# Optimization experiments

Hardware: AMD Instinct MI355X
Metric: run time of the kernel (lower is better)

## Reference

```python
import jax, jax.numpy as jnp
import numpy as np

N_STATE = 12
HID = 128
BS = 16384


def setup_inputs() -> dict:
    key = jax.random.key(0)
    ks = jax.random.split(key, 16)
    s = 0.05
    inp = {
        'state': jax.random.normal(ks[0], (BS, N_STATE), dtype=jnp.float32),
        'safe_m': jax.random.uniform(ks[1], (N_STATE,), minval=0.5, maxval=2.0, dtype=jnp.float32),
        'safe_l': -jax.random.uniform(ks[2], (N_STATE,), minval=0.5, maxval=2.0, dtype=jnp.float32),
        'W0': jax.random.normal(ks[3], (HID, N_STATE), dtype=jnp.float32) * s,
        'b0': jax.random.normal(ks[4], (HID,), dtype=jnp.float32) * s,
        'W1': jax.random.normal(ks[5], (HID, HID), dtype=jnp.float32) * s,
        'b1': jax.random.normal(ks[6], (HID,), dtype=jnp.float32) * s,
        'W2': jax.random.normal(ks[7], (HID, HID), dtype=jnp.float32) * s,
        'b2': jax.random.normal(ks[8], (HID,), dtype=jnp.float32) * s,
        'W3': jax.random.normal(ks[9], (HID, HID), dtype=jnp.float32) * s,
        'b3': jax.random.normal(ks[10], (HID,), dtype=jnp.float32) * s,
        'Wout': jax.random.normal(ks[11], (1, HID), dtype=jnp.float32) * s,
        'bout': jax.random.normal(ks[12], (1,), dtype=jnp.float32) * s,
    }
    return inp


def _linear(V, JV, W, b):
    # V: (bs, in) -> (bs, out); JV: (bs, in, n) -> (bs, out, n)
    return V @ W.T + b, jnp.einsum('oh,bhn->bon', W, JV)


def _tanh(V, JV):
    V = jnp.tanh(V)
    # diag_embed(1 - V^2) @ JV  ==  elementwise row scaling
    return V, (1.0 - V * V)[:, :, None] * JV


def reference(state, safe_m, safe_l, W0, b0, W1, b1, W2, b2, W3, b3, Wout, bout):
    bs = state.shape[0]
    x_center = (safe_m + safe_l) * 0.5            # (n,)
    x_range = (safe_m - safe_l) * 0.5             # (n,)
    x_norm = (state - x_center) / x_range         # (bs, n)

    # JV initialized to diag(1/x_range), broadcast over batch
    JV = jnp.broadcast_to(jnp.diag(1.0 / x_range), (bs, N_STATE, N_STATE))

    V, JV = _linear(x_norm, JV, W0, b0)   # input_linear
    V, JV = _tanh(V, JV)                  # input_activation
    V, JV = _linear(V, JV, W1, b1)        # layer_0_linear
    V, JV = _tanh(V, JV)                  # layer_0_activation
    V, JV = _linear(V, JV, W2, b2)        # layer_1_linear
    V, JV = _tanh(V, JV)                  # layer_1_activation
    V, JV = _linear(V, JV, W3, b3)        # layer_2_linear (no activation)
    V, JV = _linear(V, JV, Wout, bout)    # output_linear -> V:(bs,1), JV:(bs,1,n)

    # HJH = hstack(h, Jh) generalized over batch: (bs, 1 + n_state)
    return jnp.concatenate([V, JV[:, 0, :]], axis=1)
```

## Files before the change

kernel.cpp:

```cpp
#include <hip/hip_runtime.h>

#define NS  12
#define HID 128
#define SPB 8
#define RB  128

typedef __attribute__((ext_vector_type(8))) short bf8_t;
typedef __attribute__((ext_vector_type(4))) float f4_t;

#define O_W0H 0
#define O_W0L 2048
#define O_WH(i) (4096 + (i) * 16384)
#define O_WL(i) (O_WH(i) + 8192)

__device__ __forceinline__ unsigned f2bf_u(float f) {
  unsigned u = __float_as_uint(f);
  return (u + 0x7FFFu + ((u >> 16) & 1u)) >> 16;
}
__device__ __forceinline__ float bf2f(unsigned h) { return __uint_as_float(h << 16); }

__device__ __forceinline__ unsigned cvtpk(float a, float b) {
  unsigned r;
  asm("v_cvt_pk_bf16_f32 %0, %1, %2" : "=v"(r) : "v"(a), "v"(b));
  return r;
}
__device__ __forceinline__ float fast_tanh(float v) {
  float vc = fminf(fmaxf(v, -15.f), 15.f);
  float e = __expf(vc + vc);
  return (e - 1.f) * __builtin_amdgcn_rcpf(e + 1.f);
}
__device__ __forceinline__ f4_t mfma16(bf8_t a, bf8_t b, f4_t c) {
  return __builtin_amdgcn_mfma_f32_16x16x32_bf16(a, b, c, 0, 0, 0);
}

__global__ __launch_bounds__(256) void prep_w(
    const float* __restrict__ W0, const float* __restrict__ W1,
    const float* __restrict__ W2, const float* __restrict__ W3,
    unsigned* __restrict__ ws)
{
  int t = blockIdx.x * 256 + threadIdx.x;
  if (t >= 53248) return;
  int tile = t >> 9;
  int pos  = t & 511;
  int g = pos >> 7, o = (pos >> 3) & 15, j = pos & 7;

  const float* src; int kdim; unsigned hoff, loff; int lt;
  if (tile < 8) { src = W0; kdim = NS; hoff = O_W0H; loff = O_W0L; lt = tile; }
  else {
    int li = (tile - 8) >> 5;  lt = (tile - 8) & 31;
    src = (li == 0) ? W1 : (li == 1) ? W2 : W3;
    kdim = HID; hoff = O_WH(li); loff = O_WL(li);
  }
  int ks = (tile < 8) ? 0 : (lt >> 3);
  int mt = (tile < 8) ? lt : (lt & 7);
  int k = ks * 32 + g * 8 + j;
  int orow = mt * 16 + o;
  float v = (k < kdim) ? src[orow * kdim + k] : 0.f;
  unsigned h = f2bf_u(v);
  unsigned lo = f2bf_u(v - bf2f(h));
  int idx = lt * 512 + pos;
  ((unsigned short*)(ws + hoff))[idx] = (unsigned short)h;
  ((unsigned short*)(ws + loff))[idx] = (unsigned short)lo;
}

template<int KSUBS, bool ACT>
__device__ __forceinline__ void layer(
    unsigned* __restrict__ S, const unsigned* __restrict__ whi,
    const unsigned* __restrict__ wlo, const float* __restrict__ bias,
    int lane, int l15, int g, int bp, int rwave, int mwave, int mt0)
{
  f4_t acc[4][2];
  #pragma unroll
  for (int a = 0; a < 4; ++a)
    #pragma unroll
    for (int b = 0; b < 2; ++b) acc[a][b] = (f4_t){0.f, 0.f, 0.f, 0.f};

  const int aswz = (l15 & 7) << 2;
  #pragma unroll
  for (int ks = 0; ks < KSUBS; ++ks) {
    bf8_t bh[2], bl[2];
    #pragma unroll
    for (int mm = 0; mm < 2; ++mm) {
      int tb = (ks * 8 + mt0 + mm) * 256 + lane * 4;
      bh[mm] = __builtin_bit_cast(bf8_t, *(const uint4*)(whi + tb));
      bl[mm] = __builtin_bit_cast(bf8_t, *(const uint4*)(wlo + tb));
    }
    #pragma unroll
    for (int rs = 0; rs < 4; ++rs) {
      int row = rwave + rs * 16 + l15;
      int idx = row * 64 + ((ks * 16 + g * 4) ^ aswz);
      bf8_t avh = __builtin_bit_cast(bf8_t, *(const uint4*)(S + idx));
      bf8_t avl = __builtin_bit_cast(bf8_t, *(const uint4*)(S + 8192 + idx));
      #pragma unroll
      for (int mm = 0; mm < 2; ++mm) {
        acc[rs][mm] = mfma16(avh, bh[mm], acc[rs][mm]);
        acc[rs][mm] = mfma16(avh, bl[mm], acc[rs][mm]);
        acc[rs][mm] = mfma16(avl, bh[mm], acc[rs][mm]);
      }
    }
  }
  __syncthreads();

  const bool even = (lane & 1) == 0;
  #pragma unroll
  for (int rs = 0; rs < 4; ++rs) {
    #pragma unroll
    for (int mm = 0; mm < 2; ++mm) {
      int col = mwave + mm * 16 + l15;
      float bv = bias[col];
      f4_t a = acc[rs][mm];
      int rb = rwave + rs * 16 + g * 4;
      if (ACT) {
        float vb = __int_as_float(__builtin_amdgcn_ds_bpermute(bp, __float_as_int(a[0])));
        float t = fast_tanh(vb + bv);
        float s = 1.f - t * t;
        a[0] = (g == 0) ? t : a[0] * s;
        a[1] *= s; a[2] *= s; a[3] *= s;
        int wc = col >> 1;
        #pragma unroll
        for (int j = 0; j < 4; ++j) {
          float pv = __shfl_xor(a[j], 1);
          float vlo = even ? a[j] : pv;
          float vhi = even ? pv : a[j];
          unsigned wh = cvtpk(vlo, vhi);
          float rl = vlo - __uint_as_float(wh << 16);
          float rh = vhi - __uint_as_float(wh & 0xFFFF0000u);
          unsigned wl = cvtpk(rl, rh);
          if (even == (j < 2)) {
            int row = rb + j;
            int idx = row * 64 + (wc ^ ((row & 7) << 2));
            S[idx] = wh;
            S[8192 + idx] = wl;
          }
        }
      } else {
        if (g == 0) a[0] += bv;
        float* Xf = (float*)S;
        #pragma unroll
        for (int j = 0; j < 4; ++j) {
          int row = rb + j;
          Xf[row * 128 + (col ^ ((row & 7) << 2))] = a[j];
        }
      }
    }
  }
  __syncthreads();
}

__global__ __launch_bounds__(512, 4) void mlp_jac(
    const float* __restrict__ state,
    const float* __restrict__ safe_m, const float* __restrict__ safe_l,
    const unsigned* __restrict__ ws,
    const float* __restrict__ b0, const float* __restrict__ b1,
    const float* __restrict__ b2, const float* __restrict__ b3,
    const float* __restrict__ Wout, const float* __restrict__ bout,
    float* __restrict__ out, int bs)
{
  __shared__ unsigned S[16384];
  __shared__ float red[512];

  const int tid  = threadIdx.x;
  const int lane = tid & 63;
  const int wid  = tid >> 6;
  const int widR = wid >> 2;
  const int widN = wid & 3;
  const int rwave = widR * 64;
  const int mwave = widN * 32;
  const int mt0   = widN * 2;
  const int l15 = lane & 15;
  const int g   = lane >> 4;
  const int bp  = l15 * 4;
  const int s0  = blockIdx.x * SPB;

  for (int i = tid; i < RB * 16; i += 512) {
    int r = i >> 4, kp = i & 15;
    int b = r >> 4, rr = r & 15;
    int sidx = s0 + b;
    float v[2];
    #pragma unroll
    for (int t = 0; t < 2; ++t) {
      int k = kp * 2 + t;
      float val = 0.f;
      if (k < NS) {
        float m = safe_m[k], l = safe_l[k];
        float inv = 2.f / (m - l);
        if (rr == 0) {
          float sv = (sidx < bs) ? state[sidx * NS + k] : 0.f;
          val = (sv - 0.5f * (m + l)) * inv;
        } else if (k == rr - 1) val = inv;
      }
      v[t] = val;
    }
    unsigned wh = cvtpk(v[0], v[1]);
    float rl = v[0] - __uint_as_float(wh << 16);
    float rh = v[1] - __uint_as_float(wh & 0xFFFF0000u);
    unsigned wl = cvtpk(rl, rh);
    int idx = r * 64 + (kp ^ ((r & 7) << 2));
    S[idx] = wh;
    S[8192 + idx] = wl;
  }
  __syncthreads();

  layer<1, true >(S, ws + O_W0H,  ws + O_W0L,  b0, lane, l15, g, bp, rwave, mwave, mt0);
  layer<4, true >(S, ws + O_WH(0), ws + O_WL(0), b1, lane, l15, g, bp, rwave, mwave, mt0);
  layer<4, true >(S, ws + O_WH(1), ws + O_WL(1), b2, lane, l15, g, bp, rwave, mwave, mt0);
  layer<4, false>(S, ws + O_WH(2), ws + O_WL(2), b3, lane, l15, g, bp, rwave, mwave, mt0);

  {
    const float* Xf = (const float*)S;
    int r = tid & 127;
    int q = tid >> 7;
    float a = 0.f;
    #pragma unroll
    for (int kk = 0; kk < 8; ++kk) {
      int c = q * 32 + kk * 4;
      float4 x = *(const float4*)(Xf + r * 128 + (c ^ ((r & 7) << 2)));
      a = fmaf(Wout[c + 0], x.x, a);
      a = fmaf(Wout[c + 1], x.y, a);
      a = fmaf(Wout[c + 2], x.z, a);
      a = fmaf(Wout[c + 3], x.w, a);
    }
    red[tid] = a;
  }
  __syncthreads();
  if (tid < 128) {
    float tot = red[tid] + red[tid + 128] + red[tid + 256] + red[tid + 384];
    int b = tid >> 4, rr = tid & 15;
    int sidx = s0 + b;
    if (sidx < bs && rr < 13) {
      if (rr == 0) tot += bout[0];
      out[sidx * 13 + rr] = tot;
    }
  }
}

extern "C" void kernel_launch(void* const* d_in, const int* in_sizes, int n_in,
                              void* d_out, int out_size, void* d_ws, size_t ws_size,
                              hipStream_t stream)
{
  const float* state  = (const float*)d_in[0];
  const float* safe_m = (const float*)d_in[1];
  const float* safe_l = (const float*)d_in[2];
  const float* W0   = (const float*)d_in[3];
  const float* b0   = (const float*)d_in[4];
  const float* W1   = (const float*)d_in[5];
  const float* b1   = (const float*)d_in[6];
  const float* W2   = (const float*)d_in[7];
  const float* b2   = (const float*)d_in[8];
  const float* W3   = (const float*)d_in[9];
  const float* b3   = (const float*)d_in[10];
  const float* Wout = (const float*)d_in[11];
  const float* bout = (const float*)d_in[12];
  unsigned* ws = (unsigned*)d_ws;
  float* out = (float*)d_out;

  const int bs = in_sizes[0] / NS;

  prep_w<<<(53248 + 255) / 256, 256, 0, stream>>>(W0, W1, W2, W3, ws);

  const int nblocks = (bs + SPB - 1) / SPB;
  mlp_jac<<<nblocks, 512, 0, stream>>>(state, safe_m, safe_l, ws,
      b0, b1, b2, b3, Wout, bout, out, bs);
}
```

Before: 178.0 us.

## Switch to 32x32x16 MFMA with smaller blocks and double-buffered weight fragments

Replaces the 16x16x32 bf16 MFMA tiling with 32x32x16 MFMA. Blocks shrink to 4 samples (64 rows) with 256 threads, each wave owning a 32-column output tile, and prep_w repacks weights for the new fragment layout. Weight fragments for the next k-step are prefetched into a second register buffer. The intent is fewer instructions per FLOP, halved LDS per block for more resident blocks, and overlap of global weight loads with MFMA work. The cost is less weight reuse per block, since each weight fragment now covers 64 rows instead of 128.

```diff
diff --git a/kernel.cpp b/kernel.cpp
--- a/kernel.cpp
+++ b/kernel.cpp
@@ -2,15 +2,15 @@
 
 #define NS  12
 #define HID 128
-#define SPB 8
-#define RB  128
-
-typedef __attribute__((ext_vector_type(8))) short bf8_t;
-typedef __attribute__((ext_vector_type(4))) float f4_t;
+#define SPB 4
+#define RB  64
+
+typedef __attribute__((ext_vector_type(8)))  short bf8_t;
+typedef __attribute__((ext_vector_type(16))) float f16f;
 
 #define O_W0H 0
-#define O_W0L 2048
-#define O_WH(i) (4096 + (i) * 16384)
+#define O_W0L 1024
+#define O_WH(i) (2048 + (i) * 16384)
 #define O_WL(i) (O_WH(i) + 8192)
 
 __device__ __forceinline__ unsigned f2bf_u(float f) {
@@ -24,13 +24,8 @@
   asm("v_cvt_pk_bf16_f32 %0, %1, %2" : "=v"(r) : "v"(a), "v"(b));
   return r;
 }
-__device__ __forceinline__ float fast_tanh(float v) {
-  float vc = fminf(fmaxf(v, -15.f), 15.f);
-  float e = __expf(vc + vc);
-  return (e - 1.f) * __builtin_amdgcn_rcpf(e + 1.f);
-}
-__device__ __forceinline__ f4_t mfma16(bf8_t a, bf8_t b, f4_t c) {
-  return __builtin_amdgcn_mfma_f32_16x16x32_bf16(a, b, c, 0, 0, 0);
+__device__ __forceinline__ f16f mfma32(bf8_t a, bf8_t b, f16f c) {
+  return __builtin_amdgcn_mfma_f32_32x32x16_bf16(a, b, c, 0, 0, 0);
 }
 
 __global__ __launch_bounds__(256) void prep_w(
@@ -39,115 +34,124 @@
     unsigned* __restrict__ ws)
 {
   int t = blockIdx.x * 256 + threadIdx.x;
-  if (t >= 53248) return;
-  int tile = t >> 9;
-  int pos  = t & 511;
-  int g = pos >> 7, o = (pos >> 3) & 15, j = pos & 7;
+  if (t >= 25600) return;
+  int tile = t >> 8;
+  int pos  = (t & 255) * 2;
+  int ln = pos >> 3, j = pos & 7;
 
   const float* src; int kdim; unsigned hoff, loff; int lt;
-  if (tile < 8) { src = W0; kdim = NS; hoff = O_W0H; loff = O_W0L; lt = tile; }
+  if (tile < 4) { src = W0; kdim = NS; hoff = O_W0H; loff = O_W0L; lt = tile; }
   else {
-    int li = (tile - 8) >> 5;  lt = (tile - 8) & 31;
+    int li = (tile - 4) >> 5;  lt = (tile - 4) & 31;
     src = (li == 0) ? W1 : (li == 1) ? W2 : W3;
     kdim = HID; hoff = O_WH(li); loff = O_WL(li);
   }
-  int ks = (tile < 8) ? 0 : (lt >> 3);
-  int mt = (tile < 8) ? lt : (lt & 7);
-  int k = ks * 32 + g * 8 + j;
-  int orow = mt * 16 + o;
-  float v = (k < kdim) ? src[orow * kdim + k] : 0.f;
-  unsigned h = f2bf_u(v);
-  unsigned lo = f2bf_u(v - bf2f(h));
-  int idx = lt * 512 + pos;
-  ((unsigned short*)(ws + hoff))[idx] = (unsigned short)h;
-  ((unsigned short*)(ws + loff))[idx] = (unsigned short)lo;
-}
-
-template<int KSUBS, bool ACT>
+  int ks = (tile < 4) ? 0 : (lt >> 2);
+  int nt = (tile < 4) ? lt : (lt & 3);
+  int k0 = ks * 16 + (ln >> 5) * 8 + j;
+  int n  = nt * 32 + (ln & 31);
+  float v0 = (k0 < kdim)     ? src[n * kdim + k0]     : 0.f;
+  float v1 = (k0 + 1 < kdim) ? src[n * kdim + k0 + 1] : 0.f;
+  unsigned h0 = f2bf_u(v0), h1 = f2bf_u(v1);
+  unsigned l0 = f2bf_u(v0 - bf2f(h0)), l1 = f2bf_u(v1 - bf2f(h1));
+  int widx = (lt * 512 + pos) >> 1;
+  (ws + hoff)[widx] = h0 | (h1 << 16);
+  (ws + loff)[widx] = l0 | (l1 << 16);
+}
+
+template<int KSUBS, bool TANH>
 __device__ __forceinline__ void layer(
-    unsigned* __restrict__ S, const unsigned* __restrict__ whi,
-    const unsigned* __restrict__ wlo, const float* __restrict__ bias,
-    int lane, int l15, int g, int bp, int rwave, int mwave, int mt0)
-{
-  f4_t acc[4][2];
-  #pragma unroll
-  for (int a = 0; a < 4; ++a)
-    #pragma unroll
-    for (int b = 0; b < 2; ++b) acc[a][b] = (f4_t){0.f, 0.f, 0.f, 0.f};
-
-  const int aswz = (l15 & 7) << 2;
+    unsigned* __restrict__ S,
+    const unsigned* __restrict__ whi, const unsigned* __restrict__ wlo,
+    const float* __restrict__ bias, int l31, int g2, int nt, int bp)
+{
+  f16f acc[2] = {};
+  const int lane = g2 * 32 + l31;
+  const int srm = (l31 & 15) << 2;
+
+  bf8_t bh[2], bl[2];
+  {
+    int tb = nt * 256 + lane * 4;
+    bh[0] = __builtin_bit_cast(bf8_t, *(const uint4*)(whi + tb));
+    bl[0] = __builtin_bit_cast(bf8_t, *(const uint4*)(wlo + tb));
+  }
+
   #pragma unroll
   for (int ks = 0; ks < KSUBS; ++ks) {
-    bf8_t bh[2], bl[2];
-    #pragma unroll
-    for (int mm = 0; mm < 2; ++mm) {
-      int tb = (ks * 8 + mt0 + mm) * 256 + lane * 4;
-      bh[mm] = __builtin_bit_cast(bf8_t, *(const uint4*)(whi + tb));
-      bl[mm] = __builtin_bit_cast(bf8_t, *(const uint4*)(wlo + tb));
-    }
-    #pragma unroll
-    for (int rs = 0; rs < 4; ++rs) {
-      int row = rwave + rs * 16 + l15;
-      int idx = row * 64 + ((ks * 16 + g * 4) ^ aswz);
+    const int cur = ks & 1, nxt = cur ^ 1;
+    if (ks + 1 < KSUBS) {
+      int tb = ((ks + 1) * 4 + nt) * 256 + lane * 4;
+      bh[nxt] = __builtin_bit_cast(bf8_t, *(const uint4*)(whi + tb));
+      bl[nxt] = __builtin_bit_cast(bf8_t, *(const uint4*)(wlo + tb));
+    }
+    #pragma unroll
+    for (int rt = 0; rt < 2; ++rt) {
+      int m = rt * 32 + l31;
+      int idx = m * 64 + ((ks * 8 + g2 * 4) ^ srm);
       bf8_t avh = __builtin_bit_cast(bf8_t, *(const uint4*)(S + idx));
-      bf8_t avl = __builtin_bit_cast(bf8_t, *(const uint4*)(S + 8192 + idx));
-      #pragma unroll
-      for (int mm = 0; mm < 2; ++mm) {
-        acc[rs][mm] = mfma16(avh, bh[mm], acc[rs][mm]);
-        acc[rs][mm] = mfma16(avh, bl[mm], acc[rs][mm]);
-        acc[rs][mm] = mfma16(avl, bh[mm], acc[rs][mm]);
+      bf8_t avl = __builtin_bit_cast(bf8_t, *(const uint4*)(S + 4096 + idx));
+      acc[rt] = mfma32(avh, bh[cur], acc[rt]);
+      acc[rt] = mfma32(avh, bl[cur], acc[rt]);
+      acc[rt] = mfma32(avl, bh[cur], acc[rt]);
+    }
+  }
+
+  const float bv = bias[nt * 32 + l31];
+  __syncthreads();
+
+  const bool ev = (l31 & 1) == 0;
+  const int wcb = nt * 16 + (l31 >> 1);
+  #pragma unroll
+  for (int rt = 0; rt < 2; ++rt) {
+    float t0, s0, t1, s1;
+    if (TANH) {
+      float pre0 = acc[rt][0] + bv;
+      float pre8 = acc[rt][8] + bv;
+      float vb0 = __int_as_float(__builtin_amdgcn_ds_bpermute(bp, __float_as_int(pre0)));
+      float vb8 = __int_as_float(__builtin_amdgcn_ds_bpermute(bp, __float_as_int(pre8)));
+      float e0 = __expf(fminf(vb0, 15.f) * 2.f);
+      t0 = (e0 - 1.f) * __builtin_amdgcn_rcpf(e0 + 1.f);
+      s0 = fmaf(-t0, t0, 1.f);
+      float e1 = __expf(fminf(vb8, 15.f) * 2.f);
+      t1 = (e1 - 1.f) * __builtin_amdgcn_rcpf(e1 + 1.f);
+      s1 = fmaf(-t1, t1, 1.f);
+    }
+    #pragma unroll
+    for (int reg = 0; reg < 16; ++reg) {
+      float a = acc[rt][reg];
+      float v;
+      if (TANH) {
+        float ss = (reg < 8) ? s0 : s1;
+        float tt = (reg < 8) ? t0 : t1;
+        v = ((reg & 7) == 0) ? ((g2 == 0) ? tt : a * ss) : a * ss;
+      } else {
+        v = ((reg & 7) == 0) ? ((g2 == 0) ? a + bv : a) : a;
       }
-    }
-  }
-  __syncthreads();
-
-  const bool even = (lane & 1) == 0;
-  #pragma unroll
-  for (int rs = 0; rs < 4; ++rs) {
-    #pragma unroll
-    for (int mm = 0; mm < 2; ++mm) {
-      int col = mwave + mm * 16 + l15;
-      float bv = bias[col];
-      f4_t a = acc[rs][mm];
-      int rb = rwave + rs * 16 + g * 4;
-      if (ACT) {
-        float vb = __int_as_float(__builtin_amdgcn_ds_bpermute(bp, __float_as_int(a[0])));
-        float t = fast_tanh(vb + bv);
-        float s = 1.f - t * t;
-        a[0] = (g == 0) ? t : a[0] * s;
-        a[1] *= s; a[2] *= s; a[3] *= s;
-        int wc = col >> 1;
-        #pragma unroll
-        for (int j = 0; j < 4; ++j) {
-          float pv = __shfl_xor(a[j], 1);
-          float vlo = even ? a[j] : pv;
-          float vhi = even ? pv : a[j];
+      int r = rt * 32 + (reg & 3) + 8 * (reg >> 2) + 4 * g2;
+      if (TANH) {
+        float p = __shfl_xor(v, 1);
+        if ((reg & 1) == (l31 & 1)) {
+          float vlo = ev ? v : p;
+          float vhi = ev ? p : v;
           unsigned wh = cvtpk(vlo, vhi);
           float rl = vlo - __uint_as_float(wh << 16);
           float rh = vhi - __uint_as_float(wh & 0xFFFF0000u);
           unsigned wl = cvtpk(rl, rh);
-          if (even == (j < 2)) {
-            int row = rb + j;
-            int idx = row * 64 + (wc ^ ((row & 7) << 2));
-            S[idx] = wh;
-            S[8192 + idx] = wl;
-          }
+          int idx = r * 64 + (wcb ^ ((r & 15) << 2));
+          S[idx] = wh;  S[4096 + idx] = wl;
         }
       } else {
-        if (g == 0) a[0] += bv;
         float* Xf = (float*)S;
-        #pragma unroll
-        for (int j = 0; j < 4; ++j) {
-          int row = rb + j;
-          Xf[row * 128 + (col ^ ((row & 7) << 2))] = a[j];
-        }
+        int c = nt * 32 + l31;
+        int idx = r * 128 + ((c & ~3) ^ ((r & 31) << 2)) + (c & 3);
+        Xf[idx] = v;
       }
     }
   }
   __syncthreads();
 }
 
-__global__ __launch_bounds__(512, 4) void mlp_jac(
+__global__ __launch_bounds__(256, 4) void mlp_jac(
     const float* __restrict__ state,
     const float* __restrict__ safe_m, const float* __restrict__ safe_l,
     const unsigned* __restrict__ ws,
@@ -156,24 +160,19 @@
     const float* __restrict__ Wout, const float* __restrict__ bout,
     float* __restrict__ out, int bs)
 {
-  __shared__ unsigned S[16384];
-  __shared__ float red[512];
+  __shared__ unsigned S[8192];
+  __shared__ float red[256];
 
   const int tid  = threadIdx.x;
   const int lane = tid & 63;
-  const int wid  = tid >> 6;
-  const int widR = wid >> 2;
-  const int widN = wid & 3;
-  const int rwave = widR * 64;
-  const int mwave = widN * 32;
-  const int mt0   = widN * 2;
-  const int l15 = lane & 15;
-  const int g   = lane >> 4;
-  const int bp  = l15 * 4;
-  const int s0  = blockIdx.x * SPB;
-
-  for (int i = tid; i < RB * 16; i += 512) {
-    int r = i >> 4, kp = i & 15;
+  const int nt   = tid >> 6;
+  const int l31  = lane & 31;
+  const int g2   = lane >> 5;
+  const int bp   = l31 << 2;
+  const int s0   = blockIdx.x * SPB;
+
+  for (int i = tid; i < RB * 8; i += 256) {
+    int r = i >> 3, kp = i & 7;
     int b = r >> 4, rr = r & 15;
     int sidx = s0 + b;
     float v[2];
@@ -195,26 +194,27 @@
     float rl = v[0] - __uint_as_float(wh << 16);
     float rh = v[1] - __uint_as_float(wh & 0xFFFF0000u);
     unsigned wl = cvtpk(rl, rh);
-    int idx = r * 64 + (kp ^ ((r & 7) << 2));
+    int idx = r * 64 + (kp ^ ((r & 15) << 2));
     S[idx] = wh;
-    S[8192 + idx] = wl;
-  }
-  __syncthreads();
-
-  layer<1, true >(S, ws + O_W0H,  ws + O_W0L,  b0, lane, l15, g, bp, rwave, mwave, mt0);
-  layer<4, true >(S, ws + O_WH(0), ws + O_WL(0), b1, lane, l15, g, bp, rwave, mwave, mt0);
-  layer<4, true >(S, ws + O_WH(1), ws + O_WL(1), b2, lane, l15, g, bp, rwave, mwave, mt0);
-  layer<4, false>(S, ws + O_WH(2), ws + O_WL(2), b3, lane, l15, g, bp, rwave, mwave, mt0);
+    S[4096 + idx] = wl;
+  }
+  __syncthreads();
+
+  layer<1, true >(S, ws + O_W0H,   ws + O_W0L,   b0, l31, g2, nt, bp);
+  layer<8, true >(S, ws + O_WH(0), ws + O_WL(0), b1, l31, g2, nt, bp);
+  layer<8, true >(S, ws + O_WH(1), ws + O_WL(1), b2, l31, g2, nt, bp);
+  layer<8, false>(S, ws + O_WH(2), ws + O_WL(2), b3, l31, g2, nt, bp);
 
   {
     const float* Xf = (const float*)S;
-    int r = tid & 127;
-    int q = tid >> 7;
+    int r = tid & 63;
+    int q = tid >> 6;
+    int sw = (r & 31) << 2;
     float a = 0.f;
     #pragma unroll
     for (int kk = 0; kk < 8; ++kk) {
       int c = q * 32 + kk * 4;
-      float4 x = *(const float4*)(Xf + r * 128 + (c ^ ((r & 7) << 2)));
+      const float4 x = *(const float4*)(Xf + r * 128 + (c ^ sw));
       a = fmaf(Wout[c + 0], x.x, a);
       a = fmaf(Wout[c + 1], x.y, a);
       a = fmaf(Wout[c + 2], x.z, a);
@@ -223,8 +223,8 @@
     red[tid] = a;
   }
   __syncthreads();
-  if (tid < 128) {
-    float tot = red[tid] + red[tid + 128] + red[tid + 256] + red[tid + 384];
+  if (tid < 64) {
+    float tot = red[tid] + red[tid + 64] + red[tid + 128] + red[tid + 192];
     int b = tid >> 4, rr = tid & 15;
     int sidx = s0 + b;
     if (sidx < bs && rr < 13) {
@@ -256,9 +256,9 @@
 
   const int bs = in_sizes[0] / NS;
 
-  prep_w<<<(53248 + 255) / 256, 256, 0, stream>>>(W0, W1, W2, W3, ws);
+  prep_w<<<100, 256, 0, stream>>>(W0, W1, W2, W3, ws);
 
   const int nblocks = (bs + SPB - 1) / SPB;
-  mlp_jac<<<nblocks, 512, 0, stream>>>(state, safe_m, safe_l, ws,
+  mlp_jac<<<nblocks, 256, 0, stream>>>(state, safe_m, safe_l, ws,
       b0, b1, b2, b3, Wout, bout, out, bs);
 }
```

Result: no change. 175.2 us (-1.6%).
